# Kernel tuning notes

Measured on AMD Instinct MI355X. Metric: run time of the kernel, lower is better.

Reference implementation:

```python
import jax, jax.numpy as jnp
import numpy as np

HIDDEN = 768
HEADS = 12
HEAD_DIM = HIDDEN // HEADS


def setup_inputs() -> dict:
    key = jax.random.key(0)
    ks = jax.random.split(key, 6)
    B, N = 32, 577  # N = 1 CLS + 576 patches
    x = jax.random.normal(ks[0], (B, N, HIDDEN), dtype=jnp.float32)
    seg_bias = jax.random.uniform(ks[1], (B, N - 1), dtype=jnp.float32)
    w_qkv = jax.random.normal(ks[2], (HIDDEN, 3 * HIDDEN), dtype=jnp.float32) * 0.02
    b_qkv = jnp.zeros((3 * HIDDEN,), dtype=jnp.float32)
    w_proj = jax.random.normal(ks[3], (HIDDEN, HIDDEN), dtype=jnp.float32) * 0.02
    b_proj = jnp.zeros((HIDDEN,), dtype=jnp.float32)
    seg_scale = jnp.ones((), dtype=jnp.float32)
    return {"x": x, "seg_bias": seg_bias, "w_qkv": w_qkv, "b_qkv": b_qkv,
            "w_proj": w_proj, "b_proj": b_proj, "seg_scale": seg_scale}


def reference(x, seg_bias, w_qkv, b_qkv, w_proj, b_proj, seg_scale):
    B, N, _ = x.shape
    scale = HEAD_DIM ** -0.5
    qkv = x @ w_qkv + b_qkv                       # (B, N, 3*H*D)
    qkv = qkv.reshape(B, N, 3, HEADS, HEAD_DIM)
    q = qkv[:, :, 0].transpose(0, 2, 1, 3)        # (B, H, N, D)
    k = qkv[:, :, 1].transpose(0, 2, 1, 3)
    v = qkv[:, :, 2].transpose(0, 2, 1, 3)
    attn = jnp.einsum('bhqd,bhkd->bhqk', q, k) * scale  # (B, H, N, N)
    # additive seg bias on CLS-query row, patch keys only (cols 1:)
    bias = (seg_bias * seg_scale)[:, None, None, :]     # (B,1,1,N-1)
    attn = attn.at[:, :, 0:1, 1:].add(bias)
    attn = jax.nn.softmax(attn, axis=-1)
    out = jnp.einsum('bhqk,bhkd->bhqd', attn, v)        # (B, H, N, D)
    out = out.transpose(0, 2, 1, 3).reshape(B, N, HIDDEN)
    return out @ w_proj + b_proj
```

## Files before the change

kernel.cpp:

```cpp
#include <hip/hip_runtime.h>


typedef unsigned short bf16_t;
typedef __attribute__((ext_vector_type(8))) short short8;
typedef __attribute__((ext_vector_type(4))) short short4v;
typedef __attribute__((ext_vector_type(4))) float f32x4;

#define B_    32
#define N_    577
#define BN_   18464
#define HID_  768
#define NH_   12
#define HD_   64
#define QKVC_ 2304
#define NPAD_ 640
#define PB_LD 68

__device__ __forceinline__ bf16_t f2bf(float f) {
  union { float f; unsigned u; } x; x.f = f;
  unsigned r = x.u + 0x7fffu + ((x.u >> 16) & 1u);
  return (bf16_t)(r >> 16);
}

__device__ __forceinline__ unsigned cvt_pk_bf16(float a, float b) {
  unsigned r;
  asm("v_cvt_pk_bf16_f32 %0, %1, %2" : "=v"(r) : "v"(a), "v"(b));
  return r;
}

__global__ __launch_bounds__(256) void cast_kernel(const float* __restrict__ in,
                                                   bf16_t* __restrict__ out, int n4) {
  int i = blockIdx.x * 256 + threadIdx.x;
  if (i >= n4) return;
  float4 v = ((const float4*)in)[i];
  ushort4 o;
  o.x = f2bf(v.x); o.y = f2bf(v.y); o.z = f2bf(v.z); o.w = f2bf(v.w);
  ((ushort4*)out)[i] = o;
}

__global__ __launch_bounds__(256) void transpose_cast_kernel(const float* __restrict__ in,
                                                             bf16_t* __restrict__ out,
                                                             int R, int C) {
  __shared__ float tile[32][33];
  int c0 = blockIdx.x * 32, r0 = blockIdx.y * 32;
  int tx = threadIdx.x, ty = threadIdx.y;
  #pragma unroll
  for (int i = ty; i < 32; i += 8)
    tile[i][tx] = in[(size_t)(r0 + i) * C + c0 + tx];
  __syncthreads();
  #pragma unroll
  for (int i = ty; i < 32; i += 8)
    out[(size_t)(c0 + i) * R + r0 + tx] = f2bf(tile[tx][i]);
}

template <int OUT_BF16>
__global__ __launch_bounds__(256, 3) void gemm_bf16_kernel(
    const bf16_t* __restrict__ A,
    const bf16_t* __restrict__ Bt,
    const float* __restrict__ bias,
    void* __restrict__ Cout,
    int M, int Nc) {
  __shared__ bf16_t As[128 * 64];
  __shared__ bf16_t Bs[128 * 64];

  const int tid  = threadIdx.x;
  const int lane = tid & 63, w = tid >> 6;
  const int quad = lane >> 4, l16 = lane & 15;

  const int Mb = (M + 127) >> 7;
  const int Nb = Nc >> 7;
  const int np_full = Mb >> 3;
  const int rem = Mb - np_full * 8;
  int bid = blockIdx.x;
  int m_blk, n_blk;
  int body = np_full * 8 * Nb;
  if (bid < body) {
    int p = bid / (8 * Nb), local = bid % (8 * Nb);
    m_blk = p * 8 + (local & 7);
    n_blk = local >> 3;
  } else {
    int t = bid - body;
    m_blk = np_full * 8 + t % rem;
    n_blk = t / rem;
  }
  const int m0 = m_blk * 128, n0 = n_blk * 128;
  const int wm = (w >> 1) * 64, wn = (w & 1) * 64;

  f32x4 acc[4][4];
  #pragma unroll
  for (int i = 0; i < 4; ++i)
    #pragma unroll
    for (int j = 0; j < 4; ++j)
      acc[i][j] = (f32x4){0.f, 0.f, 0.f, 0.f};

  for (int kt = 0; kt < 768; kt += 64) {
    __syncthreads();
    #pragma unroll
    for (int it = 0; it < 4; ++it) {
      int gi = it * 256 + tid;
      int row = gi >> 3, chp = gi & 7;
      int ch = chp ^ (row & 7);
      int gm = m0 + row; if (gm >= M) gm = M - 1;
      __builtin_amdgcn_global_load_lds(
          (const __attribute__((address_space(1))) unsigned int*)(A + (size_t)gm * 768 + kt + ch * 8),
          (__attribute__((address_space(3))) unsigned int*)(As + gi * 8),
          16, 0, 0);
      int gn = n0 + row;
      __builtin_amdgcn_global_load_lds(
          (const __attribute__((address_space(1))) unsigned int*)(Bt + (size_t)gn * 768 + kt + ch * 8),
          (__attribute__((address_space(3))) unsigned int*)(Bs + gi * 8),
          16, 0, 0);
    }
    __syncthreads();

    #pragma unroll
    for (int ks = 0; ks < 2; ++ks) {
      short8 af[4], bfr[4];
      #pragma unroll
      for (int i = 0; i < 4; ++i) {
        int row = wm + i * 16 + l16;
        int c = ks * 4 + quad;
        af[i] = *(const short8*)(As + row * 64 + (c ^ (row & 7)) * 8);
      }
      #pragma unroll
      for (int j = 0; j < 4; ++j) {
        int row = wn + j * 16 + l16;
        int c = ks * 4 + quad;
        bfr[j] = *(const short8*)(Bs + row * 64 + (c ^ (row & 7)) * 8);
      }
      #pragma unroll
      for (int i = 0; i < 4; ++i)
        #pragma unroll
        for (int j = 0; j < 4; ++j)
          acc[i][j] = __builtin_amdgcn_mfma_f32_16x16x32_bf16(af[i], bfr[j], acc[i][j], 0, 0, 0);
    }
  }

  #pragma unroll
  for (int i = 0; i < 4; ++i) {
    int mrow_base = m0 + wm + i * 16 + quad * 4;
    #pragma unroll
    for (int j = 0; j < 4; ++j) {
      int col = n0 + wn + j * 16 + l16;
      float bs = bias[col];
      #pragma unroll
      for (int r = 0; r < 4; ++r) {
        int row = mrow_base + r;
        if (row < M) {
          float v = acc[i][j][r] + bs;
          if (OUT_BF16)
            ((bf16_t*)Cout)[(size_t)row * Nc + col] = f2bf(v);
          else
            ((float*)Cout)[(size_t)row * Nc + col] = v;
        }
      }
    }
  }
}

__global__ __launch_bounds__(256) void vt_kernel(const bf16_t* __restrict__ qkv,
                                                 bf16_t* __restrict__ vT) {
  const int t = blockIdx.x, h = blockIdx.y, b = blockIdx.z;
  const int tid = threadIdx.x;
  __shared__ bf16_t Ls[64 * 65];
  const int kv0 = t * 64;
  const bf16_t* Vp = qkv + (size_t)b * N_ * QKVC_ + 2 * HID_ + h * HD_;

  #pragma unroll
  for (int it = 0; it < 2; ++it) {
    int idx = it * 256 + tid;
    int row = idx >> 3, ch = idx & 7;
    int krow = kv0 + row; if (krow > N_ - 1) krow = N_ - 1;
    short8 v8 = *(const short8*)(Vp + (size_t)krow * QKVC_ + ch * 8);
    #pragma unroll
    for (int j = 0; j < 8; ++j)
      Ls[(ch * 8 + j) * 65 + row] = (bf16_t)v8[j];
  }
  __syncthreads();
  bf16_t* outp = vT + ((size_t)(b * NH_ + h) * HD_) * NPAD_;
  #pragma unroll
  for (int it = 0; it < 2; ++it) {
    int idx = it * 256 + tid;
    int d = idx >> 3, kc = idx & 7;
    short8 o8;
    #pragma unroll
    for (int j = 0; j < 8; ++j) {
      int p = kc * 8 + j;
      int ky = ((p & 3) << 4) | (p >> 2);
      o8[j] = (short)Ls[d * 65 + ky];
    }
    *(short8*)(outp + (size_t)d * NPAD_ + kv0 + kc * 8) = o8;
  }
}

__global__ __launch_bounds__(256) void attn_kernel(
    const bf16_t* __restrict__ qkv,
    const bf16_t* __restrict__ vT,
    const float* __restrict__ seg_bias,
    const float* __restrict__ seg_scale,
    bf16_t* __restrict__ out) {
  const int bid  = blockIdx.x;
  const int pair = bid % (B_ * NH_);
  const int qt   = bid / (B_ * NH_);
  const int h    = pair % NH_;
  const int b    = pair / NH_;
  const int tid = threadIdx.x;
  const int w = tid >> 6, lane = tid & 63;
  const int quad = lane >> 4, l16 = lane & 15;
  const int xsw = l16 & 7;

  __shared__ __align__(16) bf16_t Ks[2][64 * 64];
  __shared__ __align__(16) bf16_t Vt[2][64 * 64];
  __shared__ __align__(16) bf16_t Pb[4][32 * PB_LD];

  const bf16_t* Qbase = qkv + (size_t)b * N_ * QKVC_ + h * HD_;
  const bf16_t* Kbase = Qbase + HID_;
  const bf16_t* Vtb   = vT + ((size_t)(b * NH_ + h) * HD_) * NPAD_;

  const float ssl = seg_scale[0] * 1.44269504f;

  #pragma unroll
  for (int it = 0; it < 2; ++it) {
    int gi = it * 256 + tid;
    int row = gi >> 3;
    int ch = (gi & 7) ^ (row & 7);
    __builtin_amdgcn_global_load_lds(
        (const __attribute__((address_space(1))) unsigned int*)(Kbase + (size_t)row * QKVC_ + ch * 8),
        (__attribute__((address_space(3))) unsigned int*)(&Ks[0][0] + gi * 8), 16, 0, 0);
    __builtin_amdgcn_global_load_lds(
        (const __attribute__((address_space(1))) unsigned int*)(Vtb + (size_t)row * NPAD_ + ch * 8),
        (__attribute__((address_space(3))) unsigned int*)(&Vt[0][0] + gi * 8), 16, 0, 0);
  }

  const int q0 = qt * 128 + w * 32;
  short8 qf[2][2];
  #pragma unroll
  for (int mi = 0; mi < 2; ++mi) {
    int qr = q0 + mi * 16 + l16;
    if (qr > N_ - 1) qr = N_ - 1;
    qf[mi][0] = *(const short8*)(Qbase + (size_t)qr * QKVC_ + quad * 8);
    qf[mi][1] = *(const short8*)(Qbase + (size_t)qr * QKVC_ + 32 + quad * 8);
  }
  const float qsc = 0.125f * 1.44269504f;
  #pragma unroll
  for (int mi = 0; mi < 2; ++mi)
    #pragma unroll
    for (int c = 0; c < 2; ++c)
      #pragma unroll
      for (int j = 0; j < 8; ++j) {
        unsigned u = ((unsigned)(unsigned short)qf[mi][c][j]) << 16;
        union { unsigned u; float f; } x; x.u = u;
        qf[mi][c][j] = (short)f2bf(x.f * qsc);
      }

  const f32x4 z4 = {0.f, 0.f, 0.f, 0.f};
  f32x4 o[2][4];
  f32x4 ls[2];
  #pragma unroll
  for (int mi = 0; mi < 2; ++mi) {
    ls[mi] = z4;
    #pragma unroll
    for (int j = 0; j < 4; ++j) o[mi][j] = z4;
  }

  short8 ones;
  #pragma unroll
  for (int j = 0; j < 8; ++j) ones[j] = (short)0x3F80;

  const bool bias_wave = (qt == 0 && w == 0);
  bf16_t* pw = Pb[w];

  for (int t = 0; t < 9; ++t) {
    const int cur = t & 1;

    __builtin_amdgcn_s_barrier();
    __builtin_amdgcn_sched_barrier(0);

    {
      const int kv1 = (t + 1) * 64;
      bf16_t* ksn = &Ks[1 - cur][0];
      bf16_t* vtn = &Vt[1 - cur][0];
      #pragma unroll
      for (int it = 0; it < 2; ++it) {
        int gi = it * 256 + tid;
        int row = gi >> 3;
        int ch = (gi & 7) ^ (row & 7);
        int krow = kv1 + row; if (krow > N_ - 1) krow = N_ - 1;
        __builtin_amdgcn_global_load_lds(
            (const __attribute__((address_space(1))) unsigned int*)(Kbase + (size_t)krow * QKVC_ + ch * 8),
            (__attribute__((address_space(3))) unsigned int*)(ksn + gi * 8), 16, 0, 0);
        __builtin_amdgcn_global_load_lds(
            (const __attribute__((address_space(1))) unsigned int*)(Vtb + (size_t)row * NPAD_ + kv1 + ch * 8),
            (__attribute__((address_space(3))) unsigned int*)(vtn + gi * 8), 16, 0, 0);
      }
    }

    asm volatile("s_waitcnt vmcnt(4)" ::: "memory");
    __builtin_amdgcn_sched_barrier(0);
    __builtin_amdgcn_s_barrier();
    __builtin_amdgcn_sched_barrier(0);

    const bf16_t* ks = &Ks[cur][0];
    const bf16_t* vt = &Vt[cur][0];

    f32x4 s[2][4];
    __builtin_amdgcn_s_setprio(1);
    #pragma unroll
    for (int sub = 0; sub < 4; ++sub) {
      short8 k0 = *(const short8*)(ks + (sub * 16 + l16) * 64 + (quad ^ xsw) * 8);
      short8 k1 = *(const short8*)(ks + (sub * 16 + l16) * 64 + ((4 + quad) ^ xsw) * 8);
      #pragma unroll
      for (int mi = 0; mi < 2; ++mi) {
        s[mi][sub] = __builtin_amdgcn_mfma_f32_16x16x32_bf16(qf[mi][0], k0, z4, 0, 0, 0);
        s[mi][sub] = __builtin_amdgcn_mfma_f32_16x16x32_bf16(qf[mi][1], k1, s[mi][sub], 0, 0, 0);
      }
    }
    __builtin_amdgcn_s_setprio(0);

    if (bias_wave && quad == 0) {
      const int kv0 = t * 64;
      #pragma unroll
      for (int sub = 0; sub < 4; ++sub) {
        int key = kv0 + sub * 16 + l16;
        if (key >= 1)
          s[0][sub][0] += seg_bias[b * (N_ - 1) + key - 1] * ssl;
      }
    }

    #pragma unroll
    for (int mi = 0; mi < 2; ++mi)
      #pragma unroll
      for (int r = 0; r < 4; ++r) {
        float p0 = __builtin_amdgcn_exp2f(s[mi][0][r]);
        float p1 = __builtin_amdgcn_exp2f(s[mi][1][r]);
        float p2 = __builtin_amdgcn_exp2f(s[mi][2][r]);
        float p3 = __builtin_amdgcn_exp2f(s[mi][3][r]);
        uint2 pk;
        pk.x = cvt_pk_bf16(p0, p1);
        pk.y = cvt_pk_bf16(p2, p3);
        *(uint2*)(pw + (mi * 16 + quad * 4 + r) * PB_LD + l16 * 4) = pk;
      }

    #pragma unroll
    for (int mi = 0; mi < 2; ++mi) {
      const bf16_t* pr = pw + (mi * 16 + l16) * PB_LD + quad * 8;
      union { short8 v; short4v hv[2]; } pa0, pa1;
      pa0.hv[0] = *(const short4v*)(pr);
      pa0.hv[1] = *(const short4v*)(pr + 4);
      pa1.hv[0] = *(const short4v*)(pr + 32);
      pa1.hv[1] = *(const short4v*)(pr + 36);
      __builtin_amdgcn_s_setprio(1);
      ls[mi] = __builtin_amdgcn_mfma_f32_16x16x32_bf16(pa0.v, ones, ls[mi], 0, 0, 0);
      ls[mi] = __builtin_amdgcn_mfma_f32_16x16x32_bf16(pa1.v, ones, ls[mi], 0, 0, 0);
      #pragma unroll
      for (int ds = 0; ds < 4; ++ds) {
        short8 vb0 = *(const short8*)(vt + (ds * 16 + l16) * 64 + (quad ^ xsw) * 8);
        short8 vb1 = *(const short8*)(vt + (ds * 16 + l16) * 64 + ((4 + quad) ^ xsw) * 8);
        o[mi][ds] = __builtin_amdgcn_mfma_f32_16x16x32_bf16(pa0.v, vb0, o[mi][ds], 0, 0, 0);
        o[mi][ds] = __builtin_amdgcn_mfma_f32_16x16x32_bf16(pa1.v, vb1, o[mi][ds], 0, 0, 0);
      }
      __builtin_amdgcn_s_setprio(0);
    }
  }

  {
    asm volatile("s_waitcnt vmcnt(0)" ::: "memory");
    __builtin_amdgcn_sched_barrier(0);
    __builtin_amdgcn_s_barrier();
    __builtin_amdgcn_sched_barrier(0);

    const bf16_t* ks = &Ks[1][0];
    const bf16_t* vt = &Vt[1][0];

    short8 k0 = *(const short8*)(ks + l16 * 64 + (quad ^ xsw) * 8);
    short8 k1 = *(const short8*)(ks + l16 * 64 + ((4 + quad) ^ xsw) * 8);
    f32x4 s9[2];
    #pragma unroll
    for (int mi = 0; mi < 2; ++mi) {
      s9[mi] = __builtin_amdgcn_mfma_f32_16x16x32_bf16(qf[mi][0], k0, z4, 0, 0, 0);
      s9[mi] = __builtin_amdgcn_mfma_f32_16x16x32_bf16(qf[mi][1], k1, s9[mi], 0, 0, 0);
    }
    if (bias_wave && quad == 0 && l16 == 0)
      s9[0][0] += seg_bias[b * (N_ - 1) + (N_ - 2)] * ssl;

    #pragma unroll
    for (int mi = 0; mi < 2; ++mi)
      #pragma unroll
      for (int r = 0; r < 4; ++r) {
        float p0 = (l16 == 0) ? __builtin_amdgcn_exp2f(s9[mi][r]) : 0.f;
        uint2 pk;
        pk.x = cvt_pk_bf16(p0, 0.f);
        pk.y = 0u;
        *(uint2*)(pw + (mi * 16 + quad * 4 + r) * PB_LD + l16 * 4) = pk;
      }

    #pragma unroll
    for (int mi = 0; mi < 2; ++mi) {
      const bf16_t* pr = pw + (mi * 16 + l16) * PB_LD + quad * 8;
      union { short8 v; short4v hv[2]; } pa0;
      pa0.hv[0] = *(const short4v*)(pr);
      pa0.hv[1] = *(const short4v*)(pr + 4);
      ls[mi] = __builtin_amdgcn_mfma_f32_16x16x32_bf16(pa0.v, ones, ls[mi], 0, 0, 0);
      #pragma unroll
      for (int ds = 0; ds < 4; ++ds) {
        short8 vb0 = *(const short8*)(vt + (ds * 16 + l16) * 64 + (quad ^ xsw) * 8);
        o[mi][ds] = __builtin_amdgcn_mfma_f32_16x16x32_bf16(pa0.v, vb0, o[mi][ds], 0, 0, 0);
      }
    }
  }

  #pragma unroll
  for (int mi = 0; mi < 2; ++mi)
    #pragma unroll
    for (int r = 0; r < 4; ++r) {
      float inv = 1.0f / ls[mi][r];
      int row = q0 + mi * 16 + quad * 4 + r;
      if (row < N_) {
        size_t base = ((size_t)b * N_ + row) * HID_ + h * HD_;
        #pragma unroll
        for (int ds = 0; ds < 4; ++ds)
          out[base + ds * 16 + l16] = f2bf(o[mi][ds][r] * inv);
      }
    }
}

extern "C" void kernel_launch(void* const* d_in, const int* in_sizes, int n_in,
                              void* d_out, int out_size, void* d_ws, size_t ws_size,
                              hipStream_t stream) {
  const float* x         = (const float*)d_in[0];
  const float* seg_bias  = (const float*)d_in[1];
  const float* w_qkv     = (const float*)d_in[2];
  const float* b_qkv     = (const float*)d_in[3];
  const float* w_proj    = (const float*)d_in[4];
  const float* b_proj    = (const float*)d_in[5];
  const float* seg_scale = (const float*)d_in[6];

  char* ws = (char*)d_ws;
  bf16_t* xb     = (bf16_t*)ws;
  bf16_t* wqkvT  = (bf16_t*)(ws + 28360704);
  bf16_t* wprojT = (bf16_t*)(ws + 31899648);
  bf16_t* qkvb   = (bf16_t*)(ws + 33079296);
  bf16_t* vT     = (bf16_t*)(ws + 118161408);
  bf16_t* attnb  = xb;

  cast_kernel<<<(BN_ * HID_ / 4) / 256, 256, 0, stream>>>(x, xb, BN_ * HID_ / 4);
  dim3 tb(32, 8);
  transpose_cast_kernel<<<dim3(QKVC_ / 32, HID_ / 32), tb, 0, stream>>>(w_qkv, wqkvT, HID_, QKVC_);
  transpose_cast_kernel<<<dim3(HID_ / 32, HID_ / 32), tb, 0, stream>>>(w_proj, wprojT, HID_, HID_);

  gemm_bf16_kernel<1><<<145 * (QKVC_ / 128), 256, 0, stream>>>(
      xb, wqkvT, b_qkv, (void*)qkvb, BN_, QKVC_);

  vt_kernel<<<dim3(10, NH_, B_), 256, 0, stream>>>(qkvb, vT);

  attn_kernel<<<5 * NH_ * B_, 256, 0, stream>>>(qkvb, vT, seg_bias, seg_scale, attnb);

  gemm_bf16_kernel<0><<<145 * (HID_ / 128), 256, 0, stream>>>(
      attnb, wprojT, b_proj, d_out, BN_, HID_);
}
```

Measured before the change: 324.3 us.

## Share K/V tiles across 256 queries per block with 8-wave attention blocks

The attention kernel now runs 512-thread blocks of 8 waves that cover 256 queries. Each K/V tile staged in shared memory is therefore reused by twice as many queries, roughly halving K/V global-to-LDS traffic and barrier rounds per query. A templated body handles the last query range (512 and up) with single-16-row waves, and each wave's P buffer shrinks to 16 rows that are reused across its mi sub-tiles. In exchange there are fewer, larger blocks, which affects scheduling granularity and the balance of the tail blocks.

```diff
diff --git a/kernel.cpp b/kernel.cpp
--- a/kernel.cpp
+++ b/kernel.cpp
@@ -193,49 +193,39 @@
   }
 }
 
-__global__ __launch_bounds__(256) void attn_kernel(
-    const bf16_t* __restrict__ qkv,
-    const bf16_t* __restrict__ vT,
-    const float* __restrict__ seg_bias,
-    const float* __restrict__ seg_scale,
-    bf16_t* __restrict__ out) {
-  const int bid  = blockIdx.x;
-  const int pair = bid % (B_ * NH_);
-  const int qt   = bid / (B_ * NH_);
-  const int h    = pair % NH_;
-  const int b    = pair / NH_;
+template <int MI>
+__device__ __forceinline__ void attn_body(
+    int b, int h, int qbase,
+    const bf16_t* __restrict__ qkv, const bf16_t* __restrict__ vT,
+    const float* __restrict__ seg_bias, const float* __restrict__ seg_scale,
+    bf16_t* __restrict__ out,
+    bf16_t* Ks0, bf16_t* Ks1, bf16_t* Vt0, bf16_t* Vt1, bf16_t* PbAll) {
   const int tid = threadIdx.x;
   const int w = tid >> 6, lane = tid & 63;
   const int quad = lane >> 4, l16 = lane & 15;
   const int xsw = l16 & 7;
 
-  __shared__ __align__(16) bf16_t Ks[2][64 * 64];
-  __shared__ __align__(16) bf16_t Vt[2][64 * 64];
-  __shared__ __align__(16) bf16_t Pb[4][32 * PB_LD];
-
   const bf16_t* Qbase = qkv + (size_t)b * N_ * QKVC_ + h * HD_;
   const bf16_t* Kbase = Qbase + HID_;
   const bf16_t* Vtb   = vT + ((size_t)(b * NH_ + h) * HD_) * NPAD_;
 
   const float ssl = seg_scale[0] * 1.44269504f;
 
-  #pragma unroll
-  for (int it = 0; it < 2; ++it) {
-    int gi = it * 256 + tid;
-    int row = gi >> 3;
-    int ch = (gi & 7) ^ (row & 7);
+  {
+    int row = tid >> 3;
+    int ch = (tid & 7) ^ (row & 7);
     __builtin_amdgcn_global_load_lds(
         (const __attribute__((address_space(1))) unsigned int*)(Kbase + (size_t)row * QKVC_ + ch * 8),
-        (__attribute__((address_space(3))) unsigned int*)(&Ks[0][0] + gi * 8), 16, 0, 0);
+        (__attribute__((address_space(3))) unsigned int*)(Ks0 + tid * 8), 16, 0, 0);
     __builtin_amdgcn_global_load_lds(
         (const __attribute__((address_space(1))) unsigned int*)(Vtb + (size_t)row * NPAD_ + ch * 8),
-        (__attribute__((address_space(3))) unsigned int*)(&Vt[0][0] + gi * 8), 16, 0, 0);
-  }
-
-  const int q0 = qt * 128 + w * 32;
-  short8 qf[2][2];
-  #pragma unroll
-  for (int mi = 0; mi < 2; ++mi) {
+        (__attribute__((address_space(3))) unsigned int*)(Vt0 + tid * 8), 16, 0, 0);
+  }
+
+  const int q0 = qbase + w * (MI * 16);
+  short8 qf[MI][2];
+  #pragma unroll
+  for (int mi = 0; mi < MI; ++mi) {
     int qr = q0 + mi * 16 + l16;
     if (qr > N_ - 1) qr = N_ - 1;
     qf[mi][0] = *(const short8*)(Qbase + (size_t)qr * QKVC_ + quad * 8);
@@ -243,7 +233,7 @@
   }
   const float qsc = 0.125f * 1.44269504f;
   #pragma unroll
-  for (int mi = 0; mi < 2; ++mi)
+  for (int mi = 0; mi < MI; ++mi)
     #pragma unroll
     for (int c = 0; c < 2; ++c)
       #pragma unroll
@@ -254,10 +244,10 @@
       }
 
   const f32x4 z4 = {0.f, 0.f, 0.f, 0.f};
-  f32x4 o[2][4];
-  f32x4 ls[2];
-  #pragma unroll
-  for (int mi = 0; mi < 2; ++mi) {
+  f32x4 o[MI][4];
+  f32x4 ls[MI];
+  #pragma unroll
+  for (int mi = 0; mi < MI; ++mi) {
     ls[mi] = z4;
     #pragma unroll
     for (int j = 0; j < 4; ++j) o[mi][j] = z4;
@@ -267,8 +257,8 @@
   #pragma unroll
   for (int j = 0; j < 8; ++j) ones[j] = (short)0x3F80;
 
-  const bool bias_wave = (qt == 0 && w == 0);
-  bf16_t* pw = Pb[w];
+  const bool bias_wave = (qbase == 0 && w == 0);
+  bf16_t* pw = PbAll + w * 16 * PB_LD;
 
   for (int t = 0; t < 9; ++t) {
     const int cur = t & 1;
@@ -278,39 +268,35 @@
 
     {
       const int kv1 = (t + 1) * 64;
-      bf16_t* ksn = &Ks[1 - cur][0];
-      bf16_t* vtn = &Vt[1 - cur][0];
-      #pragma unroll
-      for (int it = 0; it < 2; ++it) {
-        int gi = it * 256 + tid;
-        int row = gi >> 3;
-        int ch = (gi & 7) ^ (row & 7);
-        int krow = kv1 + row; if (krow > N_ - 1) krow = N_ - 1;
-        __builtin_amdgcn_global_load_lds(
-            (const __attribute__((address_space(1))) unsigned int*)(Kbase + (size_t)krow * QKVC_ + ch * 8),
-            (__attribute__((address_space(3))) unsigned int*)(ksn + gi * 8), 16, 0, 0);
-        __builtin_amdgcn_global_load_lds(
-            (const __attribute__((address_space(1))) unsigned int*)(Vtb + (size_t)row * NPAD_ + kv1 + ch * 8),
-            (__attribute__((address_space(3))) unsigned int*)(vtn + gi * 8), 16, 0, 0);
-      }
-    }
-
-    asm volatile("s_waitcnt vmcnt(4)" ::: "memory");
+      bf16_t* ksn = cur ? Ks0 : Ks1;
+      bf16_t* vtn = cur ? Vt0 : Vt1;
+      int row = tid >> 3;
+      int ch = (tid & 7) ^ (row & 7);
+      int krow = kv1 + row; if (krow > N_ - 1) krow = N_ - 1;
+      __builtin_amdgcn_global_load_lds(
+          (const __attribute__((address_space(1))) unsigned int*)(Kbase + (size_t)krow * QKVC_ + ch * 8),
+          (__attribute__((address_space(3))) unsigned int*)(ksn + tid * 8), 16, 0, 0);
+      __builtin_amdgcn_global_load_lds(
+          (const __attribute__((address_space(1))) unsigned int*)(Vtb + (size_t)row * NPAD_ + kv1 + ch * 8),
+          (__attribute__((address_space(3))) unsigned int*)(vtn + tid * 8), 16, 0, 0);
+    }
+
+    asm volatile("s_waitcnt vmcnt(2)" ::: "memory");
     __builtin_amdgcn_sched_barrier(0);
     __builtin_amdgcn_s_barrier();
     __builtin_amdgcn_sched_barrier(0);
 
-    const bf16_t* ks = &Ks[cur][0];
-    const bf16_t* vt = &Vt[cur][0];
-
-    f32x4 s[2][4];
+    const bf16_t* ks = cur ? Ks1 : Ks0;
+    const bf16_t* vt = cur ? Vt1 : Vt0;
+
+    f32x4 s[MI][4];
     __builtin_amdgcn_s_setprio(1);
     #pragma unroll
     for (int sub = 0; sub < 4; ++sub) {
       short8 k0 = *(const short8*)(ks + (sub * 16 + l16) * 64 + (quad ^ xsw) * 8);
       short8 k1 = *(const short8*)(ks + (sub * 16 + l16) * 64 + ((4 + quad) ^ xsw) * 8);
       #pragma unroll
-      for (int mi = 0; mi < 2; ++mi) {
+      for (int mi = 0; mi < MI; ++mi) {
         s[mi][sub] = __builtin_amdgcn_mfma_f32_16x16x32_bf16(qf[mi][0], k0, z4, 0, 0, 0);
         s[mi][sub] = __builtin_amdgcn_mfma_f32_16x16x32_bf16(qf[mi][1], k1, s[mi][sub], 0, 0, 0);
       }
@@ -328,7 +314,7 @@
     }
 
     #pragma unroll
-    for (int mi = 0; mi < 2; ++mi)
+    for (int mi = 0; mi < MI; ++mi) {
       #pragma unroll
       for (int r = 0; r < 4; ++r) {
         float p0 = __builtin_amdgcn_exp2f(s[mi][0][r]);
@@ -338,12 +324,10 @@
         uint2 pk;
         pk.x = cvt_pk_bf16(p0, p1);
         pk.y = cvt_pk_bf16(p2, p3);
-        *(uint2*)(pw + (mi * 16 + quad * 4 + r) * PB_LD + l16 * 4) = pk;
-      }
-
-    #pragma unroll
-    for (int mi = 0; mi < 2; ++mi) {
-      const bf16_t* pr = pw + (mi * 16 + l16) * PB_LD + quad * 8;
+        *(uint2*)(pw + (quad * 4 + r) * PB_LD + l16 * 4) = pk;
+      }
+
+      const bf16_t* pr = pw + l16 * PB_LD + quad * 8;
       union { short8 v; short4v hv[2]; } pa0, pa1;
       pa0.hv[0] = *(const short4v*)(pr);
       pa0.hv[1] = *(const short4v*)(pr + 4);
@@ -369,14 +353,14 @@
     __builtin_amdgcn_s_barrier();
     __builtin_amdgcn_sched_barrier(0);
 
-    const bf16_t* ks = &Ks[1][0];
-    const bf16_t* vt = &Vt[1][0];
+    const bf16_t* ks = Ks1;
+    const bf16_t* vt = Vt1;
 
     short8 k0 = *(const short8*)(ks + l16 * 64 + (quad ^ xsw) * 8);
     short8 k1 = *(const short8*)(ks + l16 * 64 + ((4 + quad) ^ xsw) * 8);
-    f32x4 s9[2];
-    #pragma unroll
-    for (int mi = 0; mi < 2; ++mi) {
+    f32x4 s9[MI];
+    #pragma unroll
+    for (int mi = 0; mi < MI; ++mi) {
       s9[mi] = __builtin_amdgcn_mfma_f32_16x16x32_bf16(qf[mi][0], k0, z4, 0, 0, 0);
       s9[mi] = __builtin_amdgcn_mfma_f32_16x16x32_bf16(qf[mi][1], k1, s9[mi], 0, 0, 0);
     }
@@ -384,19 +368,16 @@
       s9[0][0] += seg_bias[b * (N_ - 1) + (N_ - 2)] * ssl;
 
     #pragma unroll
-    for (int mi = 0; mi < 2; ++mi)
+    for (int mi = 0; mi < MI; ++mi) {
       #pragma unroll
       for (int r = 0; r < 4; ++r) {
         float p0 = (l16 == 0) ? __builtin_amdgcn_exp2f(s9[mi][r]) : 0.f;
         uint2 pk;
         pk.x = cvt_pk_bf16(p0, 0.f);
         pk.y = 0u;
-        *(uint2*)(pw + (mi * 16 + quad * 4 + r) * PB_LD + l16 * 4) = pk;
-      }
-
-    #pragma unroll
-    for (int mi = 0; mi < 2; ++mi) {
-      const bf16_t* pr = pw + (mi * 16 + l16) * PB_LD + quad * 8;
+        *(uint2*)(pw + (quad * 4 + r) * PB_LD + l16 * 4) = pk;
+      }
+      const bf16_t* pr = pw + l16 * PB_LD + quad * 8;
       union { short8 v; short4v hv[2]; } pa0;
       pa0.hv[0] = *(const short4v*)(pr);
       pa0.hv[1] = *(const short4v*)(pr + 4);
@@ -410,7 +391,7 @@
   }
 
   #pragma unroll
-  for (int mi = 0; mi < 2; ++mi)
+  for (int mi = 0; mi < MI; ++mi)
     #pragma unroll
     for (int r = 0; r < 4; ++r) {
       float inv = 1.0f / ls[mi][r];
@@ -422,6 +403,30 @@
           out[base + ds * 16 + l16] = f2bf(o[mi][ds][r] * inv);
       }
     }
+}
+
+__global__ __launch_bounds__(512) void attn_kernel(
+    const bf16_t* __restrict__ qkv,
+    const bf16_t* __restrict__ vT,
+    const float* __restrict__ seg_bias,
+    const float* __restrict__ seg_scale,
+    bf16_t* __restrict__ out) {
+  __shared__ __align__(16) bf16_t Ks[2][64 * 64];
+  __shared__ __align__(16) bf16_t Vt[2][64 * 64];
+  __shared__ __align__(16) bf16_t Pb[8][16 * PB_LD];
+
+  const int bid = blockIdx.x;
+  if (bid < 768) {
+    const int pair = bid % 384, qblk = bid / 384;
+    attn_body<2>(pair / NH_, pair % NH_, qblk * 256,
+                 qkv, vT, seg_bias, seg_scale, out,
+                 &Ks[0][0], &Ks[1][0], &Vt[0][0], &Vt[1][0], &Pb[0][0]);
+  } else {
+    const int pair = bid - 768;
+    attn_body<1>(pair / NH_, pair % NH_, 512,
+                 qkv, vT, seg_bias, seg_scale, out,
+                 &Ks[0][0], &Ks[1][0], &Vt[0][0], &Vt[1][0], &Pb[0][0]);
+  }
 }
 
 extern "C" void kernel_launch(void* const* d_in, const int* in_sizes, int n_in,
@@ -453,7 +458,7 @@
 
   vt_kernel<<<dim3(10, NH_, B_), 256, 0, stream>>>(qkvb, vT);
 
-  attn_kernel<<<5 * NH_ * B_, 256, 0, stream>>>(qkvb, vT, seg_bias, seg_scale, attnb);
+  attn_kernel<<<1152, 512, 0, stream>>>(qkvb, vT, seg_bias, seg_scale, attnb);
 
   gemm_bf16_kernel<0><<<145 * (HID_ / 128), 256, 0, stream>>>(
       attnb, wprojT, b_proj, d_out, BN_, HID_);
```

New measurement: 302.3 us, median of 2. 6.8% less time.
